# Performance work log

Measured on AMD Instinct MI355X. Metric: run time of the kernel, lower is better.

## Reference

```python
import jax, jax.numpy as jnp
import numpy as np

D = 512
H = 8
DH = D // H
HID = int(2 * D * 4.0 * (2.0 / 3.0))  # 2730, SwiGLU hidden


def _ln(x, g, b, eps=1e-5):
    m = jnp.mean(x, axis=-1, keepdims=True)
    v = jnp.mean(jnp.square(x - m), axis=-1, keepdims=True)
    return (x - m) * jax.lax.rsqrt(v + eps) * g + b


def _cross_attn(q_tok, kv_tok, ln_q_g, ln_q_b, ln_kv_g, ln_kv_b,
                Wqkv, bqkv, Wo, bo, Wp, bp):
    # q_tok: [B,Nq,D], kv_tok: [B,Nk,D]; Wqkv: [3D,D] fused in_proj (torch layout)
    B, Nq, _ = q_tok.shape
    Nk = kv_tok.shape[1]
    qn = _ln(q_tok, ln_q_g, ln_q_b)
    kvn = _ln(kv_tok, ln_kv_g, ln_kv_b)
    Wq, Wk, Wv = Wqkv[:D], Wqkv[D:2 * D], Wqkv[2 * D:]
    bq, bk, bv = bqkv[:D], bqkv[D:2 * D], bqkv[2 * D:]
    q = (qn @ Wq.T + bq).reshape(B, Nq, H, DH).transpose(0, 2, 1, 3)
    k = (kvn @ Wk.T + bk).reshape(B, Nk, H, DH).transpose(0, 2, 1, 3)
    v = (kvn @ Wv.T + bv).reshape(B, Nk, H, DH).transpose(0, 2, 1, 3)
    scores = jnp.einsum('bhqd,bhkd->bhqk', q, k) / jnp.sqrt(jnp.asarray(DH, q.dtype))
    attn = jax.nn.softmax(scores, axis=-1)
    ctx = jnp.einsum('bhqk,bhkd->bhqd', attn, v)
    ctx = ctx.transpose(0, 2, 1, 3).reshape(B, Nq, D)
    ctx = ctx @ Wo.T + bo          # MHA out_proj
    ctx = ctx @ Wp.T + bp          # CrossAttention extra out_proj
    return q_tok + ctx             # residual (dropout/droppath identity in eval)


def setup_inputs() -> dict:
    key = jax.random.key(0)
    ks = iter(jax.random.split(key, 32))
    s = 0.02
    inp = {
        'spatial_tokens': jax.random.normal(next(ks), (4, 4096, D), jnp.float32),
        'temporal_tokens': jax.random.normal(next(ks), (4, 512, D), jnp.float32),
    }
    for p in ('s', 't'):
        inp[f'{p}_ln_q_g'] = jnp.ones((D,), jnp.float32)
        inp[f'{p}_ln_q_b'] = jnp.zeros((D,), jnp.float32)
        inp[f'{p}_ln_kv_g'] = jnp.ones((D,), jnp.float32)
        inp[f'{p}_ln_kv_b'] = jnp.zeros((D,), jnp.float32)
        inp[f'{p}_Wqkv'] = jax.random.normal(next(ks), (3 * D, D), jnp.float32) * s
        inp[f'{p}_bqkv'] = jnp.zeros((3 * D,), jnp.float32)
        inp[f'{p}_Wo'] = jax.random.normal(next(ks), (D, D), jnp.float32) * s
        inp[f'{p}_bo'] = jnp.zeros((D,), jnp.float32)
        inp[f'{p}_Wp'] = jax.random.normal(next(ks), (D, D), jnp.float32) * s
        inp[f'{p}_bp'] = jnp.zeros((D,), jnp.float32)
    inp['mix_ln_g'] = jnp.ones((2 * D,), jnp.float32)
    inp['mix_ln_b'] = jnp.zeros((2 * D,), jnp.float32)
    inp['mix_Win'] = jax.random.normal(next(ks), (2 * HID, 2 * D), jnp.float32) * s
    inp['mix_bin'] = jnp.zeros((2 * HID,), jnp.float32)
    inp['mix_Wout'] = jax.random.normal(next(ks), (D, HID), jnp.float32) * s
    inp['mix_bout'] = jnp.zeros((D,), jnp.float32)
    return inp


def reference(spatial_tokens, temporal_tokens,
              s_ln_q_g, s_ln_q_b, s_ln_kv_g, s_ln_kv_b, s_Wqkv, s_bqkv, s_Wo, s_bo, s_Wp, s_bp,
              t_ln_q_g, t_ln_q_b, t_ln_kv_g, t_ln_kv_b, t_Wqkv, t_bqkv, t_Wo, t_bo, t_Wp, t_bp,
              mix_ln_g, mix_ln_b, mix_Win, mix_bin, mix_Wout, mix_bout):
    # 'st' (spatiotemporal) mode of CrossTransformer.forward
    s_ctx = _cross_attn(spatial_tokens, temporal_tokens,
                        s_ln_q_g, s_ln_q_b, s_ln_kv_g, s_ln_kv_b,
                        s_Wqkv, s_bqkv, s_Wo, s_bo, s_Wp, s_bp)
    t_ctx = _cross_attn(temporal_tokens, spatial_tokens,
                        t_ln_q_g, t_ln_q_b, t_ln_kv_g, t_ln_kv_b,
                        t_Wqkv, t_bqkv, t_Wo, t_bo, t_Wp, t_bp)
    t_mean = jnp.mean(t_ctx, axis=1, keepdims=True)  # [B,1,D]
    base = jnp.concatenate([s_ctx, jnp.broadcast_to(t_mean, s_ctx.shape)], axis=-1)  # [B,Ns,2D]
    h = _ln(base, mix_ln_g, mix_ln_b)
    uv = h @ mix_Win.T + mix_bin            # [B,Ns,2*HID]
    u, v = uv[..., :HID], uv[..., HID:]
    fused = (jax.nn.silu(u) * v) @ mix_Wout.T + mix_bout
    return s_ctx + fused
```

## Files before the change

kernel.cpp:

```cpp
#include <hip/hip_runtime.h>
#include <stdint.h>

typedef unsigned short u16;
typedef __bf16 bf16_t;
typedef bf16_t bf16x8 __attribute__((ext_vector_type(8)));
typedef float f32x4 __attribute__((ext_vector_type(4)));

__device__ __forceinline__ u16 f2b(float f) {
  union { float f; uint32_t u; } x; x.f = f;
  uint32_t r = x.u + 0x7fffu + ((x.u >> 16) & 1u);
  return (u16)(r >> 16);
}
__device__ __forceinline__ float b2f(u16 b) {
  union { uint32_t u; float f; } x; x.u = ((uint32_t)b) << 16;
  return x.f;
}

__device__ __forceinline__ void async16(const void* g, void* l) {
  auto gp = reinterpret_cast<__attribute__((address_space(1))) unsigned int*>(
      reinterpret_cast<uintptr_t>(g));
  auto lp = reinterpret_cast<__attribute__((address_space(3))) unsigned int*>(
      reinterpret_cast<uintptr_t>(l));
  __builtin_amdgcn_global_load_lds(gp, lp, 16, 0, 0);
}

__global__ __launch_bounds__(256) void pz_gemm_bt(
    const u16* __restrict__ A, const u16* __restrict__ B,
    const float* __restrict__ bias,
    const u16* __restrict__ residB, const float* __restrict__ residF,
    u16* __restrict__ Cb, float* __restrict__ Cf,
    int M, int N, int K, int ldA, int ldB, int ldC, int ldR,
    long aSH, long bSH, long cSH, long rSH, float alpha)
{
  __shared__ __align__(16) u16 sAll[3 * 8192];

  const int tid = threadIdx.x;
  const int wave = tid >> 6, lane = tid & 63;
  const int lr = lane & 15, lg = lane >> 4;
  const int wm = wave >> 1, wn = wave & 1;
  const int z = blockIdx.z;

  const u16* Ab = A + (long)z * aSH;
  const u16* Bb = B + (long)z * bSH;
  const int m0 = blockIdx.y * 128;
  const int n0 = blockIdx.x * 128;

  const int srow = tid >> 2;
  const int sgk = (tid & 3) ^ ((tid >> 3) & 3);
  int ar0 = m0 + srow;      if (ar0 > M - 1) ar0 = M - 1;
  int ar1 = m0 + 64 + srow; if (ar1 > M - 1) ar1 = M - 1;
  int br0 = n0 + srow;      if (br0 > N - 1) br0 = N - 1;
  int br1 = n0 + 64 + srow; if (br1 > N - 1) br1 = N - 1;
  const u16* aP0 = Ab + (long)ar0 * ldA + sgk * 8;
  const u16* aP1 = Ab + (long)ar1 * ldA + sgk * 8;
  const u16* bP0 = Bb + (long)br0 * ldB + sgk * 8;
  const u16* bP1 = Bb + (long)br1 * ldB + sgk * 8;

  auto stage = [&](int buf, int k0) {
    u16* p = sAll + buf * 8192;
    async16(aP0 + k0, p + wave * 512);
    async16(aP1 + k0, p + 2048 + wave * 512);
    async16(bP0 + k0, p + 4096 + wave * 512);
    async16(bP1 + k0, p + 6144 + wave * 512);
  };

  const int swz = (lr >> 1) & 3;
  int aoff[4], boff[4];
#pragma unroll
  for (int i = 0; i < 4; ++i) {
    aoff[i] = (wm * 64 + i * 16 + lr) * 32 + ((lg ^ swz) * 8);
    boff[i] = (wn * 64 + i * 16 + lr) * 32 + ((lg ^ swz) * 8);
  }

  f32x4 acc[4][4] = {};
  const int kiters = K >> 5;

  stage(0, 0);
  if (kiters > 1) stage(1, 32);

  int cur = 0;
  for (int kt = 0; kt < kiters; ++kt) {
    if (kt + 2 < kiters) {
      const int nx = (cur + 2 >= 3) ? cur - 1 : cur + 2;
      stage(nx, (kt + 2) << 5);
    }
    if (kt + 2 < kiters)      asm volatile("s_waitcnt vmcnt(8)" ::: "memory");
    else if (kt + 1 < kiters) asm volatile("s_waitcnt vmcnt(4)" ::: "memory");
    else                      asm volatile("s_waitcnt vmcnt(0)" ::: "memory");
    __builtin_amdgcn_s_barrier();
    asm volatile("" ::: "memory");

    const u16* base = sAll + cur * 8192;
    bf16x8 af[4], bfr[4];
#pragma unroll
    for (int i = 0; i < 4; ++i) af[i] = *(const bf16x8*)(base + aoff[i]);
#pragma unroll
    for (int i = 0; i < 4; ++i) bfr[i] = *(const bf16x8*)(base + 4096 + boff[i]);
#pragma unroll
    for (int i = 0; i < 4; ++i)
#pragma unroll
      for (int j = 0; j < 4; ++j)
        acc[i][j] = __builtin_amdgcn_mfma_f32_16x16x32_bf16(af[i], bfr[j], acc[i][j], 0, 0, 0);

    asm volatile("" ::: "memory");
    __builtin_amdgcn_s_barrier();
    cur = (cur + 1 == 3) ? 0 : cur + 1;
  }

  const long coff = (long)z * cSH;
  const long roff = (long)z * rSH;
#pragma unroll
  for (int j = 0; j < 4; ++j) {
    const int n = n0 + wn * 64 + j * 16 + lr;
    if (n < N) {
      const float bv = bias ? bias[n] : 0.0f;
#pragma unroll
      for (int i = 0; i < 4; ++i) {
        const int mb = m0 + wm * 64 + i * 16 + lg * 4;
#pragma unroll
        for (int r = 0; r < 4; ++r) {
          const int m = mb + r;
          float v = alpha * acc[i][j][r] + bv;
          const long ri = roff + (long)m * ldR + n;
          if (residB) v += b2f(residB[ri]);
          if (residF) v += residF[ri];
          const long ci = coff + (long)m * ldC + n;
          if (Cb) Cb[ci] = f2b(v);
          if (Cf) Cf[ci] = v;
        }
      }
    }
  }
}

__global__ __launch_bounds__(256) void pz_sattn(
    const u16* __restrict__ Q, const u16* __restrict__ K,
    const u16* __restrict__ V, u16* __restrict__ O)
{
  __shared__ __align__(16) u16 sQ[32 * 64];
  __shared__ __align__(16) u16 sK[512 * 32];
  __shared__ float redm[32][4];
  __shared__ float reds[32][4];

  const int tid = threadIdx.x;
  const int wave = tid >> 6, lane = tid & 63;
  const int lr = lane & 15, lg = lane >> 4;
  const int z = blockIdx.z;
  const int b = z >> 3, h = z & 7;
  const int q0 = blockIdx.x * 32;

  const u16* Qb = Q + (long)b * 4096 * 512 + h * 64;
  const u16* Kb = K + (long)b * 512 * 1024 + h * 64;
  const u16* Vb = V + ((long)b * 8 + h) * (64L * 512);
  u16* Ob = O + (long)b * 4096 * 512 + h * 64;

  {
    const int qrow = wave * 8 + (lane >> 3);
    const int qcol = ((lane & 7) ^ (lane >> 3)) * 8;
    async16(Qb + (long)(q0 + qrow) * 512 + qcol, sQ + wave * 512);
  }
  const int krow = wave * 16 + (lane >> 2);
  const int kcol = ((lane & 3) ^ ((lane >> 3) & 3)) * 8;
  const u16* kP = Kb + (long)krow * 1024 + kcol;

  f32x4 acc[8][2] = {};
#pragma unroll
  for (int kk = 0; kk < 2; ++kk) {
    __syncthreads();
#pragma unroll
    for (int s = 0; s < 8; ++s)
      async16(kP + kk * 32 + (long)s * 64 * 1024, sK + s * 2048 + wave * 512);
    __builtin_amdgcn_s_waitcnt(0x0f70);
    __syncthreads();

    bf16x8 kf[8], qf[2];
#pragma unroll
    for (int kb = 0; kb < 8; ++kb) {
      const int n = wave * 128 + kb * 16 + lr;
      kf[kb] = *(const bf16x8*)(sK + n * 32 + ((lg ^ ((lr >> 1) & 3)) * 8));
    }
#pragma unroll
    for (int nq = 0; nq < 2; ++nq) {
      const int r = nq * 16 + lr;
      qf[nq] = *(const bf16x8*)(sQ + r * 64 + (((kk * 4 + lg) ^ (r & 7)) * 8));
    }
    __builtin_amdgcn_s_setprio(1);
#pragma unroll
    for (int kb = 0; kb < 8; ++kb)
#pragma unroll
      for (int nq = 0; nq < 2; ++nq)
        acc[kb][nq] = __builtin_amdgcn_mfma_f32_16x16x32_bf16(kf[kb], qf[nq], acc[kb][nq], 0, 0, 0);
    __builtin_amdgcn_s_setprio(0);
  }

  float mx0, mx1;
  {
    float m0 = acc[0][0][0], m1 = acc[0][1][0];
#pragma unroll
    for (int kb = 0; kb < 8; ++kb)
#pragma unroll
      for (int rg = 0; rg < 4; ++rg) {
        m0 = fmaxf(m0, acc[kb][0][rg]);
        m1 = fmaxf(m1, acc[kb][1][rg]);
      }
    m0 = fmaxf(m0, __shfl_xor(m0, 16, 64)); m0 = fmaxf(m0, __shfl_xor(m0, 32, 64));
    m1 = fmaxf(m1, __shfl_xor(m1, 16, 64)); m1 = fmaxf(m1, __shfl_xor(m1, 32, 64));
    mx0 = m0; mx1 = m1;
  }
  if (lane < 16) { redm[lr][wave] = mx0; redm[16 + lr][wave] = mx1; }
  __syncthreads();
  float inv[2];
#pragma unroll
  for (int nq = 0; nq < 2; ++nq) {
    const int q = nq * 16 + lr;
    const float m = fmaxf(fmaxf(redm[q][0], redm[q][1]), fmaxf(redm[q][2], redm[q][3]));
    float s = 0.0f;
#pragma unroll
    for (int kb = 0; kb < 8; ++kb)
#pragma unroll
      for (int rg = 0; rg < 4; ++rg) {
        const float e = __expf(0.125f * (acc[kb][nq][rg] - m));
        acc[kb][nq][rg] = e;
        s += e;
      }
    s += __shfl_xor(s, 16, 64);
    s += __shfl_xor(s, 32, 64);
    if (lane < 16) reds[q][wave] = s;
  }
  __syncthreads();
#pragma unroll
  for (int nq = 0; nq < 2; ++nq) {
    const int q = nq * 16 + lr;
    inv[nq] = 1.0f / (reds[q][0] + reds[q][1] + reds[q][2] + reds[q][3]);
  }

#pragma unroll
  for (int nq = 0; nq < 2; ++nq) {
    const int q = nq * 16 + lr;
#pragma unroll
    for (int kb = 0; kb < 8; ++kb) {
      ushort4 w;
      w.x = f2b(acc[kb][nq][0] * inv[nq]);
      w.y = f2b(acc[kb][nq][1] * inv[nq]);
      w.z = f2b(acc[kb][nq][2] * inv[nq]);
      w.w = f2b(acc[kb][nq][3] * inv[nq]);
      const int c16 = wave * 16 + kb * 2 + (lg >> 1);
      const int byteoff = q * 1024 + ((c16 ^ (q & 7)) * 16) + (lg & 1) * 8;
      *(ushort4*)((char*)sK + byteoff) = w;
    }
  }
  __syncthreads();

  const u16* vp = Vb + (long)(wave * 16 + lr) * 512;
  f32x4 opv[2] = {};
#pragma unroll
  for (int ks = 0; ks < 16; ++ks) {
    const bf16x8 bv = *(const bf16x8*)(vp + ks * 32 + lg * 8);
    bf16x8 pf[2];
#pragma unroll
    for (int mi = 0; mi < 2; ++mi) {
      const int r = mi * 16 + lr;
      pf[mi] = *(const bf16x8*)((char*)sK + r * 1024 + (((ks * 4 + lg) ^ (lr & 7)) * 16));
    }
    __builtin_amdgcn_s_setprio(1);
#pragma unroll
    for (int mi = 0; mi < 2; ++mi)
      opv[mi] = __builtin_amdgcn_mfma_f32_16x16x32_bf16(pf[mi], bv, opv[mi], 0, 0, 0);
    __builtin_amdgcn_s_setprio(0);
  }
#pragma unroll
  for (int mi = 0; mi < 2; ++mi)
#pragma unroll
    for (int rg = 0; rg < 4; ++rg) {
      const int q = q0 + mi * 16 + lg * 4 + rg;
      Ob[(long)q * 512 + wave * 16 + lr] = f2b(opv[mi][rg]);
    }
}

__global__ __launch_bounds__(256) void pz_tattn(
    const u16* __restrict__ Q,
    const u16* __restrict__ K,
    const u16* __restrict__ VT,
    u16* __restrict__ O)
{
  __shared__ __align__(16) u16 sQ[32 * 64];
  __shared__ __align__(16) u16 sK[512 * 32];
  __shared__ float redm[32][4];
  __shared__ float reds[32][4];
  __shared__ float m_run[32], l_run[32], alpha_sh[32];

  const int tid = threadIdx.x;
  const int wave = tid >> 6, lane = tid & 63;
  const int lr = lane & 15, lg = lane >> 4;
  const int z = blockIdx.z;
  const int b = z >> 3, h = z & 7;
  const int q0 = blockIdx.x * 32;

  const u16* Qb = Q + (long)b * 512 * 512 + h * 64;
  const u16* Kb = K + (long)b * 4096 * 1024 + h * 64;
  const u16* Vb = VT + (long)b * 512 * 4096 + (long)h * 64 * 4096;
  u16* Ob = O + (long)b * 512 * 512 + h * 64;

  if (tid < 32) { m_run[tid] = -3.0e38f; l_run[tid] = 0.0f; }

  {
    const int qrow = wave * 8 + (lane >> 3);
    const int qcol = ((lane & 7) ^ (lane >> 3)) * 8;
    async16(Qb + (long)(q0 + qrow) * 512 + qcol, sQ + wave * 512);
  }
  const int krow = wave * 16 + (lane >> 2);
  const int kcol = ((lane & 3) ^ ((lane >> 3) & 3)) * 8;

  f32x4 opv[2] = {};

  for (int kt = 0; kt < 8; ++kt) {
    const u16* kP = Kb + ((long)kt * 512 + krow) * 1024 + kcol;
    f32x4 acc[8][2] = {};
#pragma unroll
    for (int kk = 0; kk < 2; ++kk) {
      __syncthreads();
#pragma unroll
      for (int s = 0; s < 8; ++s)
        async16(kP + kk * 32 + (long)s * 64 * 1024, sK + s * 2048 + wave * 512);
      __builtin_amdgcn_s_waitcnt(0x0f70);
      __syncthreads();

      bf16x8 kf[8], qf[2];
#pragma unroll
      for (int kb = 0; kb < 8; ++kb) {
        const int n = wave * 128 + kb * 16 + lr;
        kf[kb] = *(const bf16x8*)(sK + n * 32 + ((lg ^ ((lr >> 1) & 3)) * 8));
      }
#pragma unroll
      for (int nq = 0; nq < 2; ++nq) {
        const int r = nq * 16 + lr;
        qf[nq] = *(const bf16x8*)(sQ + r * 64 + (((kk * 4 + lg) ^ (r & 7)) * 8));
      }
      __builtin_amdgcn_s_setprio(1);
#pragma unroll
      for (int kb = 0; kb < 8; ++kb)
#pragma unroll
        for (int nq = 0; nq < 2; ++nq)
          acc[kb][nq] = __builtin_amdgcn_mfma_f32_16x16x32_bf16(kf[kb], qf[nq], acc[kb][nq], 0, 0, 0);
      __builtin_amdgcn_s_setprio(0);
    }

#pragma unroll
    for (int nq = 0; nq < 2; ++nq) {
      float m = acc[0][nq][0];
#pragma unroll
      for (int kb = 0; kb < 8; ++kb)
#pragma unroll
        for (int rg = 0; rg < 4; ++rg) m = fmaxf(m, acc[kb][nq][rg]);
      m = fmaxf(m, __shfl_xor(m, 16, 64));
      m = fmaxf(m, __shfl_xor(m, 32, 64));
      if (lane < 16) redm[nq * 16 + lr][wave] = m;
    }
    __syncthreads();

#pragma unroll
    for (int nq = 0; nq < 2; ++nq) {
      const int q = nq * 16 + lr;
      const float mt = fmaxf(fmaxf(redm[q][0], redm[q][1]), fmaxf(redm[q][2], redm[q][3]));
      const float mn = fmaxf(m_run[q], mt);
      float s = 0.0f;
#pragma unroll
      for (int kb = 0; kb < 8; ++kb)
#pragma unroll
        for (int rg = 0; rg < 4; ++rg) {
          const float e = __expf(0.125f * (acc[kb][nq][rg] - mn));
          acc[kb][nq][rg] = e;
          s += e;
        }
      s += __shfl_xor(s, 16, 64);
      s += __shfl_xor(s, 32, 64);
      if (lane < 16) reds[q][wave] = s;
    }
    __syncthreads();

    if (tid < 32) {
      const int q = tid;
      const float mt = fmaxf(fmaxf(redm[q][0], redm[q][1]), fmaxf(redm[q][2], redm[q][3]));
      const float mo = m_run[q];
      const float mn = fmaxf(mo, mt);
      const float al = __expf(0.125f * (mo - mn));
      l_run[q] = l_run[q] * al + (reds[q][0] + reds[q][1] + reds[q][2] + reds[q][3]);
      m_run[q] = mn;
      alpha_sh[q] = al;
    }
#pragma unroll
    for (int nq = 0; nq < 2; ++nq) {
      const int q = nq * 16 + lr;
#pragma unroll
      for (int kb = 0; kb < 8; ++kb) {
        ushort4 w;
        w.x = f2b(acc[kb][nq][0]);
        w.y = f2b(acc[kb][nq][1]);
        w.z = f2b(acc[kb][nq][2]);
        w.w = f2b(acc[kb][nq][3]);
        const int c16 = wave * 16 + kb * 2 + (lg >> 1);
        const int byteoff = q * 1024 + ((c16 ^ (q & 7)) * 16) + (lg & 1) * 8;
        *(ushort4*)((char*)sK + byteoff) = w;
      }
    }
    __syncthreads();

#pragma unroll
    for (int mi = 0; mi < 2; ++mi)
#pragma unroll
      for (int rg = 0; rg < 4; ++rg)
        opv[mi][rg] *= alpha_sh[mi * 16 + lg * 4 + rg];

    const u16* vp = Vb + (long)(wave * 16 + lr) * 4096 + kt * 512;
#pragma unroll
    for (int ks = 0; ks < 16; ++ks) {
      const bf16x8 bv = *(const bf16x8*)(vp + ks * 32 + lg * 8);
      bf16x8 pf[2];
#pragma unroll
      for (int mi = 0; mi < 2; ++mi) {
        const int r = mi * 16 + lr;
        pf[mi] = *(const bf16x8*)((char*)sK + r * 1024 + (((ks * 4 + lg) ^ (lr & 7)) * 16));
      }
      __builtin_amdgcn_s_setprio(1);
#pragma unroll
      for (int mi = 0; mi < 2; ++mi)
        opv[mi] = __builtin_amdgcn_mfma_f32_16x16x32_bf16(pf[mi], bv, opv[mi], 0, 0, 0);
      __builtin_amdgcn_s_setprio(0);
    }
  }

#pragma unroll
  for (int mi = 0; mi < 2; ++mi)
#pragma unroll
    for (int rg = 0; rg < 4; ++rg) {
      const int qr = mi * 16 + lg * 4 + rg;
      Ob[(long)(q0 + qr) * 512 + wave * 16 + lr] = f2b(opv[mi][rg] * (1.0f / l_run[qr]));
    }
}

__global__ __launch_bounds__(256) void pz_gemm_uvgate(
    const u16* __restrict__ A, const u16* __restrict__ Bu, const u16* __restrict__ Bv,
    const float* __restrict__ biasU, const float* __restrict__ biasV,
    u16* __restrict__ G, int M, int N, int K, int ldA, int ldB, int ldG, int Npad)
{
  __shared__ __align__(16) u16 sAll[3 * 8192];

  const int tid = threadIdx.x;
  const int wave = tid >> 6, lane = tid & 63;
  const int lr = lane & 15, lg = lane >> 4;
  const int wm = wave >> 1, wn = wave & 1;
  const int m0 = blockIdx.y * 128;
  const int n0 = blockIdx.x * 64;

  const int srow = tid >> 2;
  const int sgk = (tid & 3) ^ ((tid >> 3) & 3);
  int ar0 = m0 + srow;      if (ar0 > M - 1) ar0 = M - 1;
  int ar1 = m0 + 64 + srow; if (ar1 > M - 1) ar1 = M - 1;
  int br  = n0 + srow;      if (br  > N - 1) br  = N - 1;
  const u16* aP0 = A + (long)ar0 * ldA + sgk * 8;
  const u16* aP1 = A + (long)ar1 * ldA + sgk * 8;
  const u16* uP  = Bu + (long)br * ldB + sgk * 8;
  const u16* vP  = Bv + (long)br * ldB + sgk * 8;

  auto stage = [&](int buf, int k0) {
    u16* b = sAll + buf * 8192;
    async16(aP0 + k0, b + wave * 512);
    async16(aP1 + k0, b + 2048 + wave * 512);
    async16(uP + k0, b + 4096 + wave * 512);
    async16(vP + k0, b + 6144 + wave * 512);
  };

  const int swz = (lr >> 1) & 3;
  int aoff[4], boff[2];
#pragma unroll
  for (int i = 0; i < 4; ++i) aoff[i] = (wm * 64 + i * 16 + lr) * 32 + ((lg ^ swz) * 8);
#pragma unroll
  for (int j = 0; j < 2; ++j) boff[j] = (wn * 32 + j * 16 + lr) * 32 + ((lg ^ swz) * 8);

  f32x4 aU[4][2] = {}, aV[4][2] = {};
  const int kiters = K >> 5;

  stage(0, 0);
  if (kiters > 1) stage(1, 32);

  int cur = 0;
  for (int kt = 0; kt < kiters; ++kt) {
    if (kt + 2 < kiters) {
      const int nx = (cur + 2 >= 3) ? cur - 1 : cur + 2;
      stage(nx, (kt + 2) << 5);
    }
    if (kt + 2 < kiters)      asm volatile("s_waitcnt vmcnt(8)" ::: "memory");
    else if (kt + 1 < kiters) asm volatile("s_waitcnt vmcnt(4)" ::: "memory");
    else                      asm volatile("s_waitcnt vmcnt(0)" ::: "memory");
    __builtin_amdgcn_s_barrier();
    asm volatile("" ::: "memory");

    const u16* base = sAll + cur * 8192;
    bf16x8 af[4], uf[2], vf[2];
#pragma unroll
    for (int i = 0; i < 4; ++i) af[i] = *(const bf16x8*)(base + aoff[i]);
#pragma unroll
    for (int j = 0; j < 2; ++j) uf[j] = *(const bf16x8*)(base + 4096 + boff[j]);
#pragma unroll
    for (int j = 0; j < 2; ++j) vf[j] = *(const bf16x8*)(base + 6144 + boff[j]);
#pragma unroll
    for (int i = 0; i < 4; ++i)
#pragma unroll
      for (int j = 0; j < 2; ++j) {
        aU[i][j] = __builtin_amdgcn_mfma_f32_16x16x32_bf16(af[i], uf[j], aU[i][j], 0, 0, 0);
        aV[i][j] = __builtin_amdgcn_mfma_f32_16x16x32_bf16(af[i], vf[j], aV[i][j], 0, 0, 0);
      }

    asm volatile("" ::: "memory");
    __builtin_amdgcn_s_barrier();
    cur = (cur + 1 == 3) ? 0 : cur + 1;
  }

#pragma unroll
  for (int j = 0; j < 2; ++j) {
    const int n = n0 + wn * 32 + j * 16 + lr;
    if (n < N) {
      const float bu = biasU[n], bv = biasV[n];
#pragma unroll
      for (int i = 0; i < 4; ++i) {
        const int mb = m0 + wm * 64 + i * 16 + lg * 4;
#pragma unroll
        for (int r = 0; r < 4; ++r) {
          const float u = aU[i][j][r] + bu;
          const float v = aV[i][j][r] + bv;
          G[(long)(mb + r) * ldG + n] = f2b((u / (1.0f + __expf(-u))) * v);
        }
      }
    } else if (n < Npad) {
#pragma unroll
      for (int i = 0; i < 4; ++i) {
        const int mb = m0 + wm * 64 + i * 16 + lg * 4;
#pragma unroll
        for (int r = 0; r < 4; ++r) G[(long)(mb + r) * ldG + n] = 0;
      }
    }
  }
}

__global__ __launch_bounds__(256) void pz_ln2(
    const float* __restrict__ X0, const float* __restrict__ X1,
    u16* __restrict__ O0, u16* __restrict__ O1, int split)
{
  __shared__ float sm[4], sq[4];
  const int tid = threadIdx.x;
  const long row = blockIdx.x;
  const float* x;
  u16* O;
  if (row < split) { x = X0 + row * 512; O = O0 + row * 512; }
  else             { const long r2 = row - split; x = X1 + r2 * 512; O = O1 + r2 * 512; }
  float a = x[tid], b = x[tid + 256];
  float s = a + b, q = a * a + b * b;
#pragma unroll
  for (int m = 32; m >= 1; m >>= 1) { s += __shfl_xor(s, m, 64); q += __shfl_xor(q, m, 64); }
  if ((tid & 63) == 0) { sm[tid >> 6] = s; sq[tid >> 6] = q; }
  __syncthreads();
  s = sm[0] + sm[1] + sm[2] + sm[3];
  q = sq[0] + sq[1] + sq[2] + sq[3];
  const float mean = s * (1.0f / 512.0f);
  const float rstd = rsqrtf(q * (1.0f / 512.0f) - mean * mean + 1e-5f);
  O[tid]       = f2b((a - mean) * rstd);
  O[tid + 256] = f2b((b - mean) * rstd);
}

__global__ __launch_bounds__(256) void pz_mix_ln(
    const u16* __restrict__ SC, const float* __restrict__ TM,
    const float* __restrict__ g, const float* __restrict__ b, u16* __restrict__ H)
{
  __shared__ float sm[4], sq[4];
  const int tid = threadIdx.x;
  const long row = blockIdx.x;
  const int bb = (int)(row >> 12);
  const u16* x0 = SC + row * 512;
  const float* x1 = TM + (long)bb * 512;
  float v0 = b2f(x0[tid]), v1 = b2f(x0[tid + 256]);
  float v2 = x1[tid], v3 = x1[tid + 256];
  float s = v0 + v1 + v2 + v3;
  float q = v0 * v0 + v1 * v1 + v2 * v2 + v3 * v3;
#pragma unroll
  for (int m = 32; m >= 1; m >>= 1) { s += __shfl_xor(s, m, 64); q += __shfl_xor(q, m, 64); }
  if ((tid & 63) == 0) { sm[tid >> 6] = s; sq[tid >> 6] = q; }
  __syncthreads();
  s = sm[0] + sm[1] + sm[2] + sm[3];
  q = sq[0] + sq[1] + sq[2] + sq[3];
  const float mean = s * (1.0f / 1024.0f);
  const float rstd = rsqrtf(q * (1.0f / 1024.0f) - mean * mean + 1e-5f);
  u16* hr = H + row * 1024;
  hr[tid]       = f2b((v0 - mean) * rstd * g[tid]       + b[tid]);
  hr[tid + 256] = f2b((v1 - mean) * rstd * g[tid + 256] + b[tid + 256]);
  hr[tid + 512] = f2b((v2 - mean) * rstd * g[tid + 512] + b[tid + 512]);
  hr[tid + 768] = f2b((v3 - mean) * rstd * g[tid + 768] + b[tid + 768]);
}

__global__ __launch_bounds__(256) void pz_transpose(
    const u16* __restrict__ S, u16* __restrict__ D, int Nk, int ldS, int colBase,
    long sBS, long dBS)
{
  __shared__ u16 t[64][65];
  const int z = blockIdx.z;
  const int nk0 = blockIdx.x * 64;
  const int tid = threadIdx.x;
  S += (long)blockIdx.y * sBS;
  D += (long)blockIdx.y * dBS;
  for (int i = tid; i < 4096; i += 256) {
    int r = i >> 6, d = i & 63;
    t[r][d] = S[(long)(nk0 + r) * ldS + colBase + z * 64 + d];
  }
  __syncthreads();
  for (int i = tid; i < 4096; i += 256) {
    int d = i >> 6, c = i & 63;
    D[((long)z * 64 + d) * Nk + nk0 + c] = t[c][d];
  }
}

__global__ __launch_bounds__(256) void pz_transpose_f2b(
    const float* __restrict__ S0, const float* __restrict__ S1,
    u16* __restrict__ D, int Nk, int ldS, long dBS)
{
  __shared__ u16 t[64][65];
  const float* S = blockIdx.y ? S1 : S0;
  D += (long)blockIdx.y * dBS;
  const int z = blockIdx.z;
  const int nk0 = blockIdx.x * 64;
  const int tid = threadIdx.x;
  for (int i = tid; i < 4096; i += 256) {
    int r = i >> 6, d = i & 63;
    t[r][d] = f2b(S[(long)(nk0 + r) * ldS + z * 64 + d]);
  }
  __syncthreads();
  for (int i = tid; i < 4096; i += 256) {
    int d = i >> 6, c = i & 63;
    D[((long)z * 64 + d) * Nk + nk0 + c] = t[c][d];
  }
}

__global__ __launch_bounds__(256) void pz_f2b(const float* __restrict__ s, u16* __restrict__ d, int n)
{
  int i = blockIdx.x * 256 + threadIdx.x;
  if (i < n) d[i] = f2b(s[i]);
}

__global__ __launch_bounds__(256) void pz_f2b2(
    const float* __restrict__ s0, const float* __restrict__ s1, u16* __restrict__ d, int n)
{
  const int i = blockIdx.x * 256 + threadIdx.x;
  d[i] = (i < n) ? f2b(s0[i]) : f2b(s1[i - n]);
}

__global__ __launch_bounds__(256) void pz_prep(
    const float* __restrict__ Ws, const float* __restrict__ Wt,
    const float* __restrict__ bs, const float* __restrict__ bt,
    const float* s_qg, const float* s_qb, const float* s_kg, const float* s_kb,
    const float* t_qg, const float* t_qb, const float* t_kg, const float* t_kb,
    u16* __restrict__ Wps, u16* __restrict__ Wpt, float* bps, float* bpt,
    const float* sWp, const float* s_bo, const float* s_bp,
    const float* tWp, const float* t_bo, const float* t_bp, float* bcs, float* bct,
    const float* __restrict__ Wout, u16* __restrict__ Dout)
{
  __shared__ float sb[4];
  const int id = blockIdx.x;
  if (id < 3072) {
    const int mat = (id >= 1536) ? 1 : 0;
    const int r = id - mat * 1536;
    const float* W = mat ? Wt : Ws;
    const float* bq = mat ? bt : bs;
    const float *g, *bl;
    if (!mat) { g = (r < 512) ? s_qg : s_kg; bl = (r < 512) ? s_qb : s_kb; }
    else      { g = (r < 512) ? t_qg : t_kg; bl = (r < 512) ? t_qb : t_kb; }
    u16* Wo_ = mat ? Wpt : Wps;
    float* bo_ = mat ? bpt : bps;
    float dot = 0.0f;
    for (int c = threadIdx.x; c < 512; c += 256) {
      float w = W[(long)r * 512 + c];
      Wo_[(long)r * 512 + c] = f2b(w * g[c]);
      dot += w * bl[c];
    }
#pragma unroll
    for (int m = 32; m >= 1; m >>= 1) dot += __shfl_xor(dot, m, 64);
    if ((threadIdx.x & 63) == 0) sb[threadIdx.x >> 6] = dot;
    __syncthreads();
    if (threadIdx.x == 0) bo_[r] = sb[0] + sb[1] + sb[2] + sb[3] + bq[r];
  } else if (id < 4096) {
    const int id2 = id - 3072;
    const int mat = id2 >> 9, i = id2 & 511;
    const float* W = mat ? tWp : sWp;
    const float* bo = mat ? t_bo : s_bo;
    const float* bp = mat ? t_bp : s_bp;
    float* o = mat ? bct : bcs;
    float dot = 0.0f;
    for (int j = threadIdx.x; j < 512; j += 256) dot += W[(long)i * 512 + j] * bo[j];
#pragma unroll
    for (int m = 32; m >= 1; m >>= 1) dot += __shfl_xor(dot, m, 64);
    if ((threadIdx.x & 63) == 0) sb[threadIdx.x >> 6] = dot;
    __syncthreads();
    if (threadIdx.x == 0) o[i] = sb[0] + sb[1] + sb[2] + sb[3] + bp[i];
  } else {
    const int idx = (id - 4096) * 256 + threadIdx.x;
    const int r = idx / 2816, c = idx - r * 2816;
    Dout[idx] = (c < 2730) ? f2b(Wout[(long)r * 2730 + c]) : (u16)0;
  }
}

__global__ __launch_bounds__(256) void pz_tmean(const u16* __restrict__ T, float* __restrict__ O)
{
  const int b = blockIdx.y, tc = blockIdx.x, tid = threadIdx.x;
  const u16* base = T + (long)b * 512 * 512 + (long)tc * 32 * 512;
  float s0 = 0.0f, s1 = 0.0f;
#pragma unroll 4
  for (int t = 0; t < 32; ++t) { s0 += b2f(base[t * 512 + tid]); s1 += b2f(base[t * 512 + tid + 256]); }
  atomicAdd(&O[b * 512 + tid],       s0 * (1.0f / 512.0f));
  atomicAdd(&O[b * 512 + tid + 256], s1 * (1.0f / 512.0f));
}

__global__ void pz_diag(float* __restrict__ out, long n, float val)
{
  for (long i = (long)blockIdx.x * 256 + threadIdx.x; i < n; i += (long)gridDim.x * 256)
    out[i] = val;
}

extern "C" void kernel_launch(void* const* d_in, const int* in_sizes, int n_in,
                              void* d_out, int out_size, void* d_ws, size_t ws_size,
                              hipStream_t stream)
{
  (void)in_sizes; (void)n_in;
  const float* spat   = (const float*)d_in[0];
  const float* temp   = (const float*)d_in[1];
  const float* s_qg = (const float*)d_in[2],  * s_qb = (const float*)d_in[3];
  const float* s_kg = (const float*)d_in[4],  * s_kb = (const float*)d_in[5];
  const float* s_Wqkv = (const float*)d_in[6], * s_bqkv = (const float*)d_in[7];
  const float* s_Wo = (const float*)d_in[8],  * s_bo = (const float*)d_in[9];
  const float* s_Wp = (const float*)d_in[10], * s_bp = (const float*)d_in[11];
  const float* t_qg = (const float*)d_in[12], * t_qb = (const float*)d_in[13];
  const float* t_kg = (const float*)d_in[14], * t_kb = (const float*)d_in[15];
  const float* t_Wqkv = (const float*)d_in[16], * t_bqkv = (const float*)d_in[17];
  const float* t_Wo = (const float*)d_in[18], * t_bo = (const float*)d_in[19];
  const float* t_Wp = (const float*)d_in[20], * t_bp = (const float*)d_in[21];
  const float* mix_g = (const float*)d_in[22], * mix_b = (const float*)d_in[23];
  const float* mix_Win = (const float*)d_in[24], * mix_bin = (const float*)d_in[25];
  const float* mix_Wout = (const float*)d_in[26], * mix_bout = (const float*)d_in[27];
  float* out = (float*)d_out;

  char* ws = (char*)d_ws;
  size_t off = 0;
  auto take = [&](size_t n) { void* p = ws + off; off += (n + 255) & ~(size_t)255; return p; };

  u16* wq_s  = (u16*)take(1536L * 512 * 2);
  u16* wq_t  = (u16*)take(1536L * 512 * 2);
  u16* wc_s  = (u16*)take(512L * 512 * 2);
  u16* wc_t  = (u16*)take(512L * 512 * 2);
  u16* woutp = (u16*)take(512L * 2816 * 2);
  float* bqs = (float*)take(1536L * 4);
  float* bqt = (float*)take(1536L * 4);
  float* bcs = (float*)take(512L * 4);
  float* bct = (float*)take(512L * 4);
  u16* nhat_s = (u16*)take(16384L * 512 * 2);
  u16* nhat_t = (u16*)take(2048L * 512 * 2);
  u16* q_s  = (u16*)take(16384L * 512 * 2);
  u16* kv_s = (u16*)take(2048L * 1024 * 2);
  u16* q_t  = (u16*)take(2048L * 512 * 2);
  u16* kv_t = (u16*)take(16384L * 1024 * 2);
  char* Sreg = (char*)take(16777216 + 2097152 + 4194304);
  const size_t NEED = off;

  if (ws_size < NEED) {
    pz_diag<<<2048, 256, 0, stream>>>(out, (long)out_size, (float)(ws_size >> 20));
    return;
  }

  u16* Gbig = (u16*)(ws + off);
  const bool bigG = (ws_size >= off + 16384UL * 2816 * 2);

  u16* wtT_all = (u16*)Sreg;
  u16* wpb_all = (u16*)(Sreg + 1048576);
  u16* vt_s = (u16*)Sreg;
  u16* vtc4 = (u16*)(Sreg + 2097152);
  u16* ctx_s = nhat_s;
  u16* ctx_t = nhat_t;
  u16* sctx  = q_s;
  u16* tctx  = kv_s;
  float* tmean = (float*)q_t;
  u16* hbuf  = kv_t;
  u16* gchunk = (u16*)Sreg;
  u16* winb   = (u16*)nhat_s;

  auto gemm = [&](const u16* A, const u16* B, const float* bias,
                  const u16* residB, const float* residF, u16* Cb, float* Cf,
                  int M, int N, int K, int ldA, int ldB, int ldC, int ldR,
                  long aSH, long bSH, long cSH, long rSH, int Z, float alpha) {
    dim3 g((N + 127) / 128, M / 128, Z);
    pz_gemm_bt<<<g, dim3(256), 0, stream>>>(A, B, bias, residB, residF, Cb, Cf,
        M, N, K, ldA, ldB, ldC, ldR, aSH, bSH, cSH, rSH, alpha);
  };

  pz_prep<<<9728, 256, 0, stream>>>(s_Wqkv, t_Wqkv, s_bqkv, t_bqkv,
      s_qg, s_qb, s_kg, s_kb, t_qg, t_qb, t_kg, t_kb, wq_s, wq_t, bqs, bqt,
      s_Wp, s_bo, s_bp, t_Wp, t_bo, t_bp, bcs, bct, mix_Wout, woutp);
  pz_transpose_f2b<<<dim3(8, 2, 8), 256, 0, stream>>>(s_Wo, t_Wo, wtT_all, 512, 512, 262144);
  pz_f2b2<<<2048, 256, 0, stream>>>(s_Wp, t_Wp, wpb_all, 512 * 512);
  gemm(wpb_all, wtT_all, nullptr, nullptr, nullptr, wc_s, nullptr,
       512, 512, 512, 512, 512, 512, 0, 262144, 262144, 262144, 0, 2, 1.0f);

  pz_ln2<<<18432, 256, 0, stream>>>(spat, temp, nhat_s, nhat_t, 16384);

  gemm(nhat_s, wq_s,           bqs,       nullptr, nullptr, q_s,  nullptr,
       16384, 512,  512, 512, 512, 512,  0, 0,0,0,0, 1, 1.0f);
  gemm(nhat_t, wq_s + 512*512, bqs + 512, nullptr, nullptr, kv_s, nullptr,
       2048,  1024, 512, 512, 512, 1024, 0, 0,0,0,0, 1, 1.0f);
  gemm(nhat_t, wq_t,           bqt,       nullptr, nullptr, q_t,  nullptr,
       2048,  512,  512, 512, 512, 512,  0, 0,0,0,0, 1, 1.0f);
  gemm(nhat_s, wq_t + 512*512, bqt + 512, nullptr, nullptr, kv_t, nullptr,
       16384, 1024, 512, 512, 512, 1024, 0, 0,0,0,0, 1, 1.0f);

  pz_transpose<<<dim3(8, 4, 8), 256, 0, stream>>>(kv_s, vt_s, 512, 1024, 512,
      512L * 1024, 8L * 64 * 512);
  pz_transpose<<<dim3(64, 4, 8), 256, 0, stream>>>(kv_t, vtc4, 4096, 1024, 512,
      4096L * 1024, 512L * 4096);

  pz_sattn<<<dim3(128, 1, 32), 256, 0, stream>>>(q_s, kv_s, vt_s, ctx_s);
  pz_tattn<<<dim3(16, 1, 32), 256, 0, stream>>>(q_t, kv_t, vtc4, ctx_t);

  gemm(ctx_s, wc_s, bcs, nullptr, spat, sctx, nullptr,
       16384, 512, 512, 512, 512, 512, 512, 0,0,0,0, 1, 1.0f);
  gemm(ctx_t, wc_t, bct, nullptr, temp, tctx, nullptr,
       2048,  512, 512, 512, 512, 512, 512, 0,0,0,0, 1, 1.0f);

  (void)hipMemsetAsync(tmean, 0, 4L * 512 * sizeof(float), stream);
  pz_tmean<<<dim3(16, 4), 256, 0, stream>>>(tctx, tmean);
  pz_mix_ln<<<16384, 256, 0, stream>>>(sctx, tmean, mix_g, mix_b, hbuf);

  pz_f2b<<<21840, 256, 0, stream>>>(mix_Win, winb, 5460 * 1024);

  if (bigG) {
    pz_gemm_uvgate<<<dim3(44, 128), 256, 0, stream>>>(hbuf, winb, winb + 2730L * 1024,
        mix_bin, mix_bin + 2730, Gbig, 16384, 2730, 1024, 1024, 1024, 2816, 2816);
    gemm(Gbig, woutp, mix_bout, sctx, nullptr, nullptr, out,
         16384, 512, 2816, 2816, 2816, 512, 512, 0,0,0,0, 1, 1.0f);
  } else {
    for (int c = 0; c < 4; ++c) {
      const u16* Ah = hbuf + (long)c * 4096 * 1024;
      pz_gemm_uvgate<<<dim3(44, 32), 256, 0, stream>>>(Ah, winb, winb + 2730L * 1024,
          mix_bin, mix_bin + 2730, gchunk, 4096, 2730, 1024, 1024, 1024, 2816, 2816);
      gemm(gchunk, woutp, mix_bout, sctx + (long)c * 4096 * 512, nullptr, nullptr,
           out + (long)c * 4096 * 512,
           4096, 512, 2816, 2816, 2816, 512, 512, 0,0,0,0, 1, 1.0f);
    }
  }
}
```

Before: 819.3 us.

## Merge Q and KV projections per input into single wide GEMMs, fuse weight cast

The prep kernel now groups weight rows by which normalized input they multiply, so each token set (spatial and temporal) gets one N=1536 GEMM producing its Q for one attention and its K/V for the other. The attention kernels take row strides so they can read Q and K directly out of the interleaved qkv buffers. The standalone mix_Win bf16 conversion is folded into the mix layernorm launch as extra blocks. This cuts GEMM launches and re-reads of the normalized activations, and removes one kernel launch, at the cost of strided Q/K loads and more complex buffer aliasing.

Measured after the change: 794.9 us (median of 2 runs). 3.0% less time.

```diff
diff --git a/kernel.cpp b/kernel.cpp
--- a/kernel.cpp
+++ b/kernel.cpp
@@ -135,7 +135,7 @@
 
 __global__ __launch_bounds__(256) void pz_sattn(
     const u16* __restrict__ Q, const u16* __restrict__ K,
-    const u16* __restrict__ V, u16* __restrict__ O)
+    const u16* __restrict__ V, u16* __restrict__ O, int ldQ, int ldK)
 {
   __shared__ __align__(16) u16 sQ[32 * 64];
   __shared__ __align__(16) u16 sK[512 * 32];
@@ -149,19 +149,19 @@
   const int b = z >> 3, h = z & 7;
   const int q0 = blockIdx.x * 32;
 
-  const u16* Qb = Q + (long)b * 4096 * 512 + h * 64;
-  const u16* Kb = K + (long)b * 512 * 1024 + h * 64;
+  const u16* Qb = Q + (long)b * 4096 * ldQ + h * 64;
+  const u16* Kb = K + (long)b * 512 * ldK + h * 64;
   const u16* Vb = V + ((long)b * 8 + h) * (64L * 512);
   u16* Ob = O + (long)b * 4096 * 512 + h * 64;
 
   {
     const int qrow = wave * 8 + (lane >> 3);
     const int qcol = ((lane & 7) ^ (lane >> 3)) * 8;
-    async16(Qb + (long)(q0 + qrow) * 512 + qcol, sQ + wave * 512);
+    async16(Qb + (long)(q0 + qrow) * ldQ + qcol, sQ + wave * 512);
   }
   const int krow = wave * 16 + (lane >> 2);
   const int kcol = ((lane & 3) ^ ((lane >> 3) & 3)) * 8;
-  const u16* kP = Kb + (long)krow * 1024 + kcol;
+  const u16* kP = Kb + (long)krow * ldK + kcol;
 
   f32x4 acc[8][2] = {};
 #pragma unroll
@@ -169,7 +169,7 @@
     __syncthreads();
 #pragma unroll
     for (int s = 0; s < 8; ++s)
-      async16(kP + kk * 32 + (long)s * 64 * 1024, sK + s * 2048 + wave * 512);
+      async16(kP + kk * 32 + (long)s * 64 * ldK, sK + s * 2048 + wave * 512);
     __builtin_amdgcn_s_waitcnt(0x0f70);
     __syncthreads();
 
@@ -278,10 +278,9 @@
 }
 
 __global__ __launch_bounds__(256) void pz_tattn(
-    const u16* __restrict__ Q,
-    const u16* __restrict__ K,
+    const u16* __restrict__ Q, const u16* __restrict__ K,
     const u16* __restrict__ VT,
-    u16* __restrict__ O)
+    u16* __restrict__ O, int ldQ, int ldK)
 {
   __shared__ __align__(16) u16 sQ[32 * 64];
   __shared__ __align__(16) u16 sK[512 * 32];
@@ -296,8 +295,8 @@
   const int b = z >> 3, h = z & 7;
   const int q0 = blockIdx.x * 32;
 
-  const u16* Qb = Q + (long)b * 512 * 512 + h * 64;
-  const u16* Kb = K + (long)b * 4096 * 1024 + h * 64;
+  const u16* Qb = Q + (long)b * 512 * ldQ + h * 64;
+  const u16* Kb = K + (long)b * 4096 * ldK + h * 64;
   const u16* Vb = VT + (long)b * 512 * 4096 + (long)h * 64 * 4096;
   u16* Ob = O + (long)b * 512 * 512 + h * 64;
 
@@ -306,7 +305,7 @@
   {
     const int qrow = wave * 8 + (lane >> 3);
     const int qcol = ((lane & 7) ^ (lane >> 3)) * 8;
-    async16(Qb + (long)(q0 + qrow) * 512 + qcol, sQ + wave * 512);
+    async16(Qb + (long)(q0 + qrow) * ldQ + qcol, sQ + wave * 512);
   }
   const int krow = wave * 16 + (lane >> 2);
   const int kcol = ((lane & 3) ^ ((lane >> 3) & 3)) * 8;
@@ -314,14 +313,14 @@
   f32x4 opv[2] = {};
 
   for (int kt = 0; kt < 8; ++kt) {
-    const u16* kP = Kb + ((long)kt * 512 + krow) * 1024 + kcol;
+    const u16* kP = Kb + ((long)kt * 512 + krow) * ldK + kcol;
     f32x4 acc[8][2] = {};
 #pragma unroll
     for (int kk = 0; kk < 2; ++kk) {
       __syncthreads();
 #pragma unroll
       for (int s = 0; s < 8; ++s)
-        async16(kP + kk * 32 + (long)s * 64 * 1024, sK + s * 2048 + wave * 512);
+        async16(kP + kk * 32 + (long)s * 64 * ldK, sK + s * 2048 + wave * 512);
       __builtin_amdgcn_s_waitcnt(0x0f70);
       __syncthreads();
 
@@ -567,12 +566,18 @@
   O[tid + 256] = f2b((b - mean) * rstd);
 }
 
-__global__ __launch_bounds__(256) void pz_mix_ln(
+__global__ __launch_bounds__(256) void pz_mix_ln_f2b(
     const u16* __restrict__ SC, const float* __restrict__ TM,
-    const float* __restrict__ g, const float* __restrict__ b, u16* __restrict__ H)
+    const float* __restrict__ g, const float* __restrict__ b, u16* __restrict__ H,
+    const float* __restrict__ Wsrc, u16* __restrict__ Wdst)
 {
   __shared__ float sm[4], sq[4];
   const int tid = threadIdx.x;
+  if (blockIdx.x >= 16384) {
+    const int i = (blockIdx.x - 16384) * 256 + tid;
+    Wdst[i] = f2b(Wsrc[i]);
+    return;
+  }
   const long row = blockIdx.x;
   const int bb = (int)(row >> 12);
   const u16* x0 = SC + row * 512;
@@ -638,12 +643,6 @@
   }
 }
 
-__global__ __launch_bounds__(256) void pz_f2b(const float* __restrict__ s, u16* __restrict__ d, int n)
-{
-  int i = blockIdx.x * 256 + threadIdx.x;
-  if (i < n) d[i] = f2b(s[i]);
-}
-
 __global__ __launch_bounds__(256) void pz_f2b2(
     const float* __restrict__ s0, const float* __restrict__ s1, u16* __restrict__ d, int n)
 {
@@ -656,7 +655,7 @@
     const float* __restrict__ bs, const float* __restrict__ bt,
     const float* s_qg, const float* s_qb, const float* s_kg, const float* s_kb,
     const float* t_qg, const float* t_qb, const float* t_kg, const float* t_kb,
-    u16* __restrict__ Wps, u16* __restrict__ Wpt, float* bps, float* bpt,
+    u16* __restrict__ wA, u16* __restrict__ wB, float* bA, float* bB,
     const float* sWp, const float* s_bo, const float* s_bp,
     const float* tWp, const float* t_bo, const float* t_bp, float* bcs, float* bct,
     const float* __restrict__ Wout, u16* __restrict__ Dout)
@@ -671,8 +670,9 @@
     const float *g, *bl;
     if (!mat) { g = (r < 512) ? s_qg : s_kg; bl = (r < 512) ? s_qb : s_kb; }
     else      { g = (r < 512) ? t_qg : t_kg; bl = (r < 512) ? t_qb : t_kb; }
-    u16* Wo_ = mat ? Wpt : Wps;
-    float* bo_ = mat ? bpt : bps;
+    const bool toA = (mat == 0) == (r < 512);
+    u16* Wo_ = toA ? wA : wB;
+    float* bo_ = toA ? bA : bB;
     float dot = 0.0f;
     for (int c = threadIdx.x; c < 512; c += 256) {
       float w = W[(long)r * 512 + c];
@@ -748,21 +748,19 @@
   size_t off = 0;
   auto take = [&](size_t n) { void* p = ws + off; off += (n + 255) & ~(size_t)255; return p; };
 
-  u16* wq_s  = (u16*)take(1536L * 512 * 2);
-  u16* wq_t  = (u16*)take(1536L * 512 * 2);
+  u16* wA    = (u16*)take(1536L * 512 * 2);
+  u16* wB    = (u16*)take(1536L * 512 * 2);
   u16* wc_s  = (u16*)take(512L * 512 * 2);
   u16* wc_t  = (u16*)take(512L * 512 * 2);
   u16* woutp = (u16*)take(512L * 2816 * 2);
-  float* bqs = (float*)take(1536L * 4);
-  float* bqt = (float*)take(1536L * 4);
+  float* bA  = (float*)take(1536L * 4);
+  float* bB  = (float*)take(1536L * 4);
   float* bcs = (float*)take(512L * 4);
   float* bct = (float*)take(512L * 4);
   u16* nhat_s = (u16*)take(16384L * 512 * 2);
   u16* nhat_t = (u16*)take(2048L * 512 * 2);
-  u16* q_s  = (u16*)take(16384L * 512 * 2);
-  u16* kv_s = (u16*)take(2048L * 1024 * 2);
-  u16* q_t  = (u16*)take(2048L * 512 * 2);
-  u16* kv_t = (u16*)take(16384L * 1024 * 2);
+  u16* qkv_s = (u16*)take(16384L * 1536 * 2);
+  u16* qkv_t = (u16*)take(2048L * 1536 * 2);
   char* Sreg = (char*)take(16777216 + 2097152 + 4194304);
   const size_t NEED = off;
 
@@ -780,10 +778,10 @@
   u16* vtc4 = (u16*)(Sreg + 2097152);
   u16* ctx_s = nhat_s;
   u16* ctx_t = nhat_t;
-  u16* sctx  = q_s;
-  u16* tctx  = kv_s;
-  float* tmean = (float*)q_t;
-  u16* hbuf  = kv_t;
+  u16* sctx  = qkv_s;
+  u16* hbuf  = qkv_s + 16384L * 512;
+  u16* tctx  = qkv_t;
+  float* tmean = (float*)(qkv_t + 2048L * 512);
   u16* gchunk = (u16*)Sreg;
   u16* winb   = (u16*)nhat_s;
 
@@ -797,7 +795,7 @@
   };
 
   pz_prep<<<9728, 256, 0, stream>>>(s_Wqkv, t_Wqkv, s_bqkv, t_bqkv,
-      s_qg, s_qb, s_kg, s_kb, t_qg, t_qb, t_kg, t_kb, wq_s, wq_t, bqs, bqt,
+      s_qg, s_qb, s_kg, s_kb, t_qg, t_qb, t_kg, t_kb, wA, wB, bA, bB,
       s_Wp, s_bo, s_bp, t_Wp, t_bo, t_bp, bcs, bct, mix_Wout, woutp);
   pz_transpose_f2b<<<dim3(8, 2, 8), 256, 0, stream>>>(s_Wo, t_Wo, wtT_all, 512, 512, 262144);
   pz_f2b2<<<2048, 256, 0, stream>>>(s_Wp, t_Wp, wpb_all, 512 * 512);
@@ -806,22 +804,18 @@
 
   pz_ln2<<<18432, 256, 0, stream>>>(spat, temp, nhat_s, nhat_t, 16384);
 
-  gemm(nhat_s, wq_s,           bqs,       nullptr, nullptr, q_s,  nullptr,
-       16384, 512,  512, 512, 512, 512,  0, 0,0,0,0, 1, 1.0f);
-  gemm(nhat_t, wq_s + 512*512, bqs + 512, nullptr, nullptr, kv_s, nullptr,
-       2048,  1024, 512, 512, 512, 1024, 0, 0,0,0,0, 1, 1.0f);
-  gemm(nhat_t, wq_t,           bqt,       nullptr, nullptr, q_t,  nullptr,
-       2048,  512,  512, 512, 512, 512,  0, 0,0,0,0, 1, 1.0f);
-  gemm(nhat_s, wq_t + 512*512, bqt + 512, nullptr, nullptr, kv_t, nullptr,
-       16384, 1024, 512, 512, 512, 1024, 0, 0,0,0,0, 1, 1.0f);
-
-  pz_transpose<<<dim3(8, 4, 8), 256, 0, stream>>>(kv_s, vt_s, 512, 1024, 512,
-      512L * 1024, 8L * 64 * 512);
-  pz_transpose<<<dim3(64, 4, 8), 256, 0, stream>>>(kv_t, vtc4, 4096, 1024, 512,
-      4096L * 1024, 512L * 4096);
-
-  pz_sattn<<<dim3(128, 1, 32), 256, 0, stream>>>(q_s, kv_s, vt_s, ctx_s);
-  pz_tattn<<<dim3(16, 1, 32), 256, 0, stream>>>(q_t, kv_t, vtc4, ctx_t);
+  gemm(nhat_s, wA, bA, nullptr, nullptr, qkv_s, nullptr,
+       16384, 1536, 512, 512, 512, 1536, 0, 0,0,0,0, 1, 1.0f);
+  gemm(nhat_t, wB, bB, nullptr, nullptr, qkv_t, nullptr,
+       2048,  1536, 512, 512, 512, 1536, 0, 0,0,0,0, 1, 1.0f);
+
+  pz_transpose<<<dim3(8, 4, 8), 256, 0, stream>>>(qkv_t, vt_s, 512, 1536, 1024,
+      512L * 1536, 8L * 64 * 512);
+  pz_transpose<<<dim3(64, 4, 8), 256, 0, stream>>>(qkv_s, vtc4, 4096, 1536, 1024,
+      4096L * 1536, 512L * 4096);
+
+  pz_sattn<<<dim3(128, 1, 32), 256, 0, stream>>>(qkv_s, qkv_t + 512, vt_s, ctx_s, 1536, 1536);
+  pz_tattn<<<dim3(16, 1, 32), 256, 0, stream>>>(qkv_t, qkv_s + 512, vtc4, ctx_t, 1536, 1536);
 
   gemm(ctx_s, wc_s, bcs, nullptr, spat, sctx, nullptr,
        16384, 512, 512, 512, 512, 512, 512, 0,0,0,0, 1, 1.0f);
@@ -830,9 +824,8 @@
 
   (void)hipMemsetAsync(tmean, 0, 4L * 512 * sizeof(float), stream);
   pz_tmean<<<dim3(16, 4), 256, 0, stream>>>(tctx, tmean);
-  pz_mix_ln<<<16384, 256, 0, stream>>>(sctx, tmean, mix_g, mix_b, hbuf);
-
-  pz_f2b<<<21840, 256, 0, stream>>>(mix_Win, winb, 5460 * 1024);
+  pz_mix_ln_f2b<<<38224, 256, 0, stream>>>(sctx, tmean, mix_g, mix_b, hbuf,
+      mix_Win, winb);
 
   if (bigG) {
     pz_gemm_uvgate<<<dim3(44, 128), 256, 0, stream>>>(hbuf, winb, winb + 2730L * 1024,
```
